# Kernel optimization log

Hardware: AMD Instinct MI355X
Metric: run time of the kernel (lower is better)

Reference implementation:

```python
import jax, jax.numpy as jnp
import numpy as np
from jax import lax

B, N, D, H, T = 32, 128, 512, 512, 31
INI = 0.01


def setup_inputs() -> dict:
    key = jax.random.key(0)
    ks = jax.random.split(key, 16)
    xav_dh = float(np.sqrt(2.0 / (D + H)))
    xav_hh = float(np.sqrt(2.0 / (H + H)))
    u = lambda k, s, a: jax.random.uniform(k, s, jnp.float32, -a, a)
    return {
        "attn_mem": jax.random.normal(ks[0], (B, N, D), jnp.float32),
        "mem_sizes": jax.random.randint(ks[1], (B,), 64, N + 1),
        "lstm_in": jax.random.normal(ks[2], (B, T, D), jnp.float32),
        "init_h": u(ks[3], (1, H), INI),
        "init_c": u(ks[4], (1, H), INI),
        "init_i": u(ks[5], (D,), 0.1),
        "w_ih": jax.random.normal(ks[6], (4 * H, D), jnp.float32) * xav_dh,
        "w_hh": jax.random.normal(ks[7], (4 * H, H), jnp.float32) * xav_hh,
        "b_ih": u(ks[8], (4 * H,), INI),
        "b_hh": u(ks[9], (4 * H,), INI),
        "attn_wm": jax.random.normal(ks[10], (D, H), jnp.float32) * xav_dh,
        "attn_wq": jax.random.normal(ks[11], (H, H), jnp.float32) * xav_hh,
        "attn_v": u(ks[12], (H,), INI),
        "hop_wm": jax.random.normal(ks[13], (D, H), jnp.float32) * xav_dh,
        "hop_wq": jax.random.normal(ks[14], (H, H), jnp.float32) * xav_hh,
        "hop_v": u(ks[15], (H,), INI),
    }


def _attention_score(feat, query, v, w):
    # feat: [B,N,H], query: [B,Tq,H] -> [B,Tq,N]
    q = jnp.einsum("bth,hk->btk", query, w)
    s = jnp.tanh(feat[:, None, :, :] + q[:, :, None, :])  # [B,Tq,N,H]
    return jnp.einsum("btnh,h->btn", s, v)


def _attention(feat, query, v, w, mask):
    score = _attention_score(feat, query, v, w)
    score = jnp.where(mask[:, None, :], score, -1e18)
    norm = jax.nn.softmax(score, axis=-1)
    return jnp.einsum("btn,bnh->bth", norm, feat)


def _lstm(x, h0, c0, w_ih, w_hh, b_ih, b_hh):
    # x: [T,B,D]; h0,c0: [B,H]; pytorch gate order i,f,g,o
    def step(carry, xt):
        h, c = carry
        g = xt @ w_ih.T + h @ w_hh.T + b_ih + b_hh
        i, f, gg, o = jnp.split(g, 4, axis=-1)
        c = jax.nn.sigmoid(f) * c + jax.nn.sigmoid(i) * jnp.tanh(gg)
        h = jax.nn.sigmoid(o) * jnp.tanh(c)
        return (h, c), h
    _, ys = lax.scan(step, (h0, c0), x)
    return ys  # [T,B,H]


def reference(attn_mem, mem_sizes, lstm_in, init_h, init_c, init_i,
              w_ih, w_hh, b_ih, b_hh, attn_wm, attn_wq, attn_v,
              hop_wm, hop_wq, hop_v, n_hop=1):
    bs, n, d = attn_mem.shape
    attn_feat = attn_mem @ attn_wm  # [B,N,H]
    hop_feat = attn_mem @ hop_wm   # [B,N,H]
    h0 = jnp.broadcast_to(init_h[0], (bs, init_h.shape[1]))
    c0 = jnp.broadcast_to(init_c[0], (bs, init_c.shape[1]))
    x = jnp.concatenate([jnp.broadcast_to(init_i, (bs, 1, d)), lstm_in], axis=1)
    query = _lstm(jnp.transpose(x, (1, 0, 2)), h0, c0, w_ih, w_hh, b_ih, b_hh)
    query = jnp.transpose(query, (1, 0, 2))  # [B,Tq,H]
    mask = jnp.arange(n)[None, :] < mem_sizes[:, None]  # [B,N]
    for _ in range(n_hop):
        query = _attention(hop_feat, query, hop_v, hop_wq, mask)
    return _attention_score(attn_feat, query, attn_v, attn_wq)
```

## Files before the change

### kernel.cpp

```cpp
#include <hip/hip_runtime.h>

typedef unsigned short u16;
typedef unsigned int u32;
typedef unsigned long long u64;
typedef __bf16 bf16x8 __attribute__((ext_vector_type(8)));
typedef float f32x4 __attribute__((ext_vector_type(4)));

__device__ __forceinline__ float b2f(u16 u) {
    unsigned int x = ((unsigned int)u) << 16;
    return __builtin_bit_cast(float, x);
}
__device__ __forceinline__ u16 f2b(float f) {
    unsigned int u = __builtin_bit_cast(unsigned int, f);
    unsigned int r = (u + 0x7FFFu + ((u >> 16) & 1u)) >> 16;
    return (u16)r;
}
__device__ __forceinline__ unsigned int pack2(float a, float b) {
    return (unsigned int)f2b(a) | ((unsigned int)f2b(b) << 16);
}
__device__ __forceinline__ float fast_rcp(float x) { return __builtin_amdgcn_rcpf(x); }
__device__ __forceinline__ float fast_tanh(float x) {
    float e = __expf(2.f * x);
    return 1.f - 2.f * fast_rcp(e + 1.f);
}
__device__ __forceinline__ float fast_sig(float x) {
    float e = __expf(-x);
    return fast_rcp(1.f + e);
}

#define FLAG_STRIDE 32

__launch_bounds__(256)
__global__ void k_prep(const float* __restrict__ attn_mem, u16* __restrict__ amem_bf,
                       const float* __restrict__ w_ih, u16* __restrict__ wih_bf,
                       const float* __restrict__ w_hh, u16* __restrict__ whh_bf,
                       const float* __restrict__ lstm_in, const float* __restrict__ init_i,
                       u16* __restrict__ xfull,
                       const float* s0, const float* s1, const float* s2, const float* s3,
                       u16* d0, u16* d1, u16* d2, u16* d3,
                       unsigned int* __restrict__ flags) {
    __shared__ float tile[32][33];
    int bid = blockIdx.x;
    int tid = threadIdx.x;
    if (bid == 0 && tid < 64)
        __hip_atomic_store(&flags[tid * FLAG_STRIDE], 0u, __ATOMIC_RELAXED,
                           __HIP_MEMORY_SCOPE_AGENT);
    if (bid < 4096) {
        const float* s;
        u16* d;
        int i;
        if (bid < 2048) { s = attn_mem; d = amem_bf; i = bid * 256 + tid; }
        else if (bid < 3072) { s = w_ih; d = wih_bf; i = (bid - 2048) * 256 + tid; }
        else { s = w_hh; d = whh_bf; i = (bid - 3072) * 256 + tid; }
        float4 a = ((const float4*)s)[i];
        uint2 p;
        p.x = pack2(a.x, a.y);
        p.y = pack2(a.z, a.w);
        ((uint2*)d)[i] = p;
    } else if (bid < 4608) {
        int idx = (bid - 4096) * 256 + tid;
        int c = idx & 127;
        int t = (idx >> 7) & 31;
        int b = idx >> 12;
        const float4* src = (t == 0) ? ((const float4*)init_i) + c
                                     : ((const float4*)lstm_in) + ((b * 31 + (t - 1)) * 128 + c);
        float4 a = *src;
        uint2 p;
        p.x = pack2(a.x, a.y);
        p.y = pack2(a.z, a.w);
        ((uint2*)xfull)[idx] = p;
    } else {
        int local = bid - 4608;
        int z = local >> 8, rem = local & 255;
        int by = (rem >> 4) * 32, bx = (rem & 15) * 32;
        const float* s;
        u16* d;
        switch (z) {
            case 0: s = s0; d = d0; break;
            case 1: s = s1; d = d1; break;
            case 2: s = s2; d = d2; break;
            default: s = s3; d = d3; break;
        }
        int tx = tid & 31, ty = tid >> 5;
        for (int i = 0; i < 32; i += 8) tile[ty + i][tx] = s[(by + ty + i) * 512 + bx + tx];
        __syncthreads();
        for (int i = 0; i < 32; i += 8) d[(bx + ty + i) * 512 + by + tx] = f2b(tile[tx][ty + i]);
    }
}

__launch_bounds__(256)
__global__ void k_mid(const u16* __restrict__ xfull, const u16* __restrict__ wih,
                      float* __restrict__ xw,
                      const float* __restrict__ b_ih, const float* __restrict__ b_hh,
                      const u16* __restrict__ amem,
                      const u16* __restrict__ WmT_hop, const u16* __restrict__ WmT_attn,
                      u16* __restrict__ hop_feat, u16* __restrict__ attn_feat) {
    __shared__ u16 As[64][40];
    __shared__ u16 Bs[64][40];
    int id = blockIdx.x;
    const u16 *A, *Bt;
    float* Cf = nullptr;
    u16* Cb = nullptr;
    const float *bias1 = nullptr, *bias2 = nullptr;
    int m0, n0, GN;
    if (id < 512) {
        A = xfull; Bt = wih; GN = 2048;
        m0 = (id >> 5) * 64; n0 = (id & 31) * 64;
        Cf = xw; bias1 = b_ih; bias2 = b_hh;
    } else {
        int local = id - 512;
        A = amem; GN = 512;
        if (local < 512) { Bt = WmT_hop; Cb = hop_feat; }
        else { Bt = WmT_attn; Cb = attn_feat; local -= 512; }
        m0 = (local >> 3) * 64; n0 = (local & 7) * 64;
    }
    int tid = threadIdx.x;
    int lane = tid & 63, w = tid >> 6;
    int wm = w >> 1, wn = w & 1;
    int l15 = lane & 15, quad = lane >> 4;
    f32x4 acc[2][2] = {};
    int ar = tid >> 2, ac = (tid & 3) * 8;
    const u16* Ap = A + (m0 + ar) * 512 + ac;
    const u16* Bp = Bt + (n0 + ar) * 512 + ac;
    for (int kt = 0; kt < 16; ++kt) {
        uint4 av = *(const uint4*)(Ap + kt * 32);
        uint4 bv = *(const uint4*)(Bp + kt * 32);
        __syncthreads();
        *(uint4*)&As[ar][ac] = av;
        *(uint4*)&Bs[ar][ac] = bv;
        __syncthreads();
        bf16x8 a0 = *(const bf16x8*)&As[wm * 32 + l15][quad * 8];
        bf16x8 a1 = *(const bf16x8*)&As[wm * 32 + 16 + l15][quad * 8];
        bf16x8 b0 = *(const bf16x8*)&Bs[wn * 32 + l15][quad * 8];
        bf16x8 b1 = *(const bf16x8*)&Bs[wn * 32 + 16 + l15][quad * 8];
        acc[0][0] = __builtin_amdgcn_mfma_f32_16x16x32_bf16(a0, b0, acc[0][0], 0, 0, 0);
        acc[0][1] = __builtin_amdgcn_mfma_f32_16x16x32_bf16(a0, b1, acc[0][1], 0, 0, 0);
        acc[1][0] = __builtin_amdgcn_mfma_f32_16x16x32_bf16(a1, b0, acc[1][0], 0, 0, 0);
        acc[1][1] = __builtin_amdgcn_mfma_f32_16x16x32_bf16(a1, b1, acc[1][1], 0, 0, 0);
    }
    for (int ai = 0; ai < 2; ++ai)
        for (int bi = 0; bi < 2; ++bi) {
            int row = m0 + wm * 32 + ai * 16 + quad * 4;
            int col = n0 + wn * 32 + bi * 16 + l15;
            if (Cb) {
                for (int r = 0; r < 4; ++r) Cb[(row + r) * GN + col] = f2b(acc[ai][bi][r]);
            } else {
                float bias = bias1[col] + bias2[col];
                for (int r = 0; r < 4; ++r) Cf[(row + r) * GN + col] = acc[ai][bi][r] + bias;
            }
        }
}

template <bool BF16OUT>
__launch_bounds__(256)
__global__ void k_gemm(const u16* __restrict__ A, const u16* __restrict__ Bt,
                       void* __restrict__ Cv, int GN,
                       const float* __restrict__ bias1, const float* __restrict__ bias2) {
    __shared__ u16 As[64][40];
    __shared__ u16 Bs[64][40];
    int m0 = blockIdx.y * 64, n0 = blockIdx.x * 64;
    int tid = threadIdx.x;
    int lane = tid & 63, w = tid >> 6;
    int wm = w >> 1, wn = w & 1;
    int l15 = lane & 15, quad = lane >> 4;
    f32x4 acc[2][2] = {};
    int ar = tid >> 2, ac = (tid & 3) * 8;
    const u16* Ap = A + (m0 + ar) * 512 + ac;
    const u16* Bp = Bt + (n0 + ar) * 512 + ac;
    for (int kt = 0; kt < 16; ++kt) {
        uint4 av = *(const uint4*)(Ap + kt * 32);
        uint4 bv = *(const uint4*)(Bp + kt * 32);
        __syncthreads();
        *(uint4*)&As[ar][ac] = av;
        *(uint4*)&Bs[ar][ac] = bv;
        __syncthreads();
        bf16x8 a0 = *(const bf16x8*)&As[wm * 32 + l15][quad * 8];
        bf16x8 a1 = *(const bf16x8*)&As[wm * 32 + 16 + l15][quad * 8];
        bf16x8 b0 = *(const bf16x8*)&Bs[wn * 32 + l15][quad * 8];
        bf16x8 b1 = *(const bf16x8*)&Bs[wn * 32 + 16 + l15][quad * 8];
        acc[0][0] = __builtin_amdgcn_mfma_f32_16x16x32_bf16(a0, b0, acc[0][0], 0, 0, 0);
        acc[0][1] = __builtin_amdgcn_mfma_f32_16x16x32_bf16(a0, b1, acc[0][1], 0, 0, 0);
        acc[1][0] = __builtin_amdgcn_mfma_f32_16x16x32_bf16(a1, b0, acc[1][0], 0, 0, 0);
        acc[1][1] = __builtin_amdgcn_mfma_f32_16x16x32_bf16(a1, b1, acc[1][1], 0, 0, 0);
    }
    for (int ai = 0; ai < 2; ++ai)
        for (int bi = 0; bi < 2; ++bi) {
            int row = m0 + wm * 32 + ai * 16 + quad * 4;
            int col = n0 + wn * 32 + bi * 16 + l15;
            float bias = 0.f;
            if (bias1) bias = bias1[col] + bias2[col];
            if constexpr (BF16OUT) {
                u16* C = (u16*)Cv;
                for (int r = 0; r < 4; ++r) C[(row + r) * GN + col] = f2b(acc[ai][bi][r] + bias);
            } else {
                float* C = (float*)Cv;
                for (int r = 0; r < 4; ++r) C[(row + r) * GN + col] = acc[ai][bi][r] + bias;
            }
        }
}

__launch_bounds__(256, 1)
__global__ void k_lstm4(const u16* __restrict__ w_hh_bf, const float* __restrict__ xw,
                        const float* __restrict__ init_h, const float* __restrict__ init_c,
                        const u16* __restrict__ wq_hop_T, float* __restrict__ qbuf,
                        u64* __restrict__ hbuf, unsigned int* __restrict__ flags) {
    __shared__ u16 Bw[32][520];
    __shared__ u16 Ah[32][520];
    __shared__ float gl[32][33];
    __shared__ u16 gbuf[32][8];
    __shared__ u16 Wq[16][520];
    int tid = threadIdx.x;
    int k0 = blockIdx.x * 8;
    int lane = tid & 63, w = tid >> 6;
    int mi = w >> 1, ni = w & 1;
    int l15 = lane & 15, quad = lane >> 4;
    int row = tid >> 3, seg = tid & 7;
    {
        int j = (row >> 3) * 512 + k0 + (row & 7);
        const uint4* src = (const uint4*)(w_hh_bf + j * 512);
        for (int i = 0; i < 8; ++i)
            *(uint4*)&Bw[row][(seg + 8 * i) * 8] = src[seg + 8 * i];
    }
    if (row < 16) {
        if (row < 8) {
            const uint4* src = (const uint4*)(wq_hop_T + (k0 + row) * 512);
            for (int i = 0; i < 8; ++i)
                *(uint4*)&Wq[row][(seg + 8 * i) * 8] = src[seg + 8 * i];
        } else {
            uint4 z = {0, 0, 0, 0};
            for (int i = 0; i < 8; ++i)
                *(uint4*)&Wq[row][(seg + 8 * i) * 8] = z;
        }
    }
    for (int i = 0; i < 8; ++i) {
        int col = (seg + 8 * i) * 8;
        float4 f0 = *(const float4*)(init_h + col);
        float4 f1 = *(const float4*)(init_h + col + 4);
        uint4 p;
        p.x = pack2(f0.x, f0.y);
        p.y = pack2(f0.z, f0.w);
        p.z = pack2(f1.x, f1.y);
        p.w = pack2(f1.z, f1.w);
        *(uint4*)&Ah[row][col] = p;
    }
    float c = init_c[k0 + seg];
    float xcur0, xcur1, xcur2, xcur3;
    {
        const float* p = xw + (row << 5) * 2048 + k0 + seg;
        xcur0 = p[0]; xcur1 = p[512]; xcur2 = p[1024]; xcur3 = p[1536];
    }
    __syncthreads();
    for (int t = 0; t < 32; ++t) {
        f32x4 acc = {};
#pragma unroll
        for (int kc = 0; kc < 16; ++kc) {
            bf16x8 a = *(const bf16x8*)&Ah[mi * 16 + l15][kc * 32 + quad * 8];
            bf16x8 b = *(const bf16x8*)&Bw[ni * 16 + l15][kc * 32 + quad * 8];
            acc = __builtin_amdgcn_mfma_f32_16x16x32_bf16(a, b, acc, 0, 0, 0);
        }
        {
            int r0 = mi * 16 + quad * 4, col = ni * 16 + l15;
            for (int r = 0; r < 4; ++r) gl[r0 + r][col] = acc[r];
        }
        __syncthreads();
        int b = row, kg = k0 + seg;
        float gi = gl[b][seg] + xcur0;
        float gf = gl[b][8 + seg] + xcur1;
        float gg = gl[b][16 + seg] + xcur2;
        float go = gl[b][24 + seg] + xcur3;
        float cnew = fast_sig(gf) * c + fast_sig(gi) * fast_tanh(gg);
        c = cnew;
        float h = fast_sig(go) * fast_tanh(cnew);
        u16 hb = f2b(h);
        gbuf[b][seg] = hb;
        __syncthreads();
        if (tid < 64) {
            int b2 = tid >> 1, half = tid & 1;
            u64 v = *(const u64*)&gbuf[b2][half * 4];
            u64* dst = hbuf + (t & 1) * 4096 + blockIdx.x * 64 + tid;
            __hip_atomic_store(dst, v, __ATOMIC_RELAXED, __HIP_MEMORY_SCOPE_AGENT);
            __builtin_amdgcn_s_waitcnt(0);
            if (tid == 0)
                __hip_atomic_store(&flags[blockIdx.x * FLAG_STRIDE], (unsigned int)(t + 1),
                                   __ATOMIC_RELAXED, __HIP_MEMORY_SCOPE_AGENT);
            while (true) {
                unsigned int f = __hip_atomic_load(&flags[tid * FLAG_STRIDE],
                                                   __ATOMIC_RELAXED, __HIP_MEMORY_SCOPE_AGENT);
                if (__ballot(f > (unsigned int)t) == ~0ull) break;
                __builtin_amdgcn_s_sleep(1);
            }
        } else if (t > 0 && w <= 2) {
            int mt = w - 1;
            f32x4 acc2 = {};
#pragma unroll
            for (int kc = 0; kc < 16; ++kc) {
                bf16x8 a = *(const bf16x8*)&Ah[mt * 16 + l15][kc * 32 + quad * 8];
                bf16x8 bq = *(const bf16x8*)&Wq[l15][kc * 32 + quad * 8];
                acc2 = __builtin_amdgcn_mfma_f32_16x16x32_bf16(a, bq, acc2, 0, 0, 0);
            }
            if (l15 < 8) {
                int bidx = mt * 16 + quad * 4;
                for (int r = 0; r < 4; ++r)
                    qbuf[(((bidx + r) << 5) + (t - 1)) * 512 + k0 + l15] = acc2[r];
            }
        }
        __syncthreads();
        int tn = (t < 31) ? t + 1 : 31;
        float xn0, xn1, xn2, xn3;
        {
            const float* p = xw + ((row << 5) + tn) * 2048 + k0 + seg;
            xn0 = p[0]; xn1 = p[512]; xn2 = p[1024]; xn3 = p[1536];
        }
        {
            const u64* src = hbuf + (t & 1) * 4096;
#pragma unroll
            for (int i = 0; i < 8; ++i) {
                int bid2 = seg + 8 * i;
                u64 v0 = __hip_atomic_load(&src[bid2 * 64 + row * 2], __ATOMIC_RELAXED,
                                           __HIP_MEMORY_SCOPE_AGENT);
                u64 v1 = __hip_atomic_load(&src[bid2 * 64 + row * 2 + 1], __ATOMIC_RELAXED,
                                           __HIP_MEMORY_SCOPE_AGENT);
                *(u64*)&Ah[row][bid2 * 8] = v0;
                *(u64*)&Ah[row][bid2 * 8 + 4] = v1;
            }
        }
        __syncthreads();
        xcur0 = xn0; xcur1 = xn1; xcur2 = xn2; xcur3 = xn3;
    }
    if (w == 1 || w == 2) {
        int mt = w - 1;
        f32x4 acc2 = {};
#pragma unroll
        for (int kc = 0; kc < 16; ++kc) {
            bf16x8 a = *(const bf16x8*)&Ah[mt * 16 + l15][kc * 32 + quad * 8];
            bf16x8 bq = *(const bf16x8*)&Wq[l15][kc * 32 + quad * 8];
            acc2 = __builtin_amdgcn_mfma_f32_16x16x32_bf16(a, bq, acc2, 0, 0, 0);
        }
        if (l15 < 8) {
            int bidx = mt * 16 + quad * 4;
            for (int r = 0; r < 4; ++r)
                qbuf[(((bidx + r) << 5) + 31) * 512 + k0 + l15] = acc2[r];
        }
    }
}

__launch_bounds__(256)
__global__ void k_hop(const u16* __restrict__ feat, const float* __restrict__ q,
                      const float* __restrict__ v, const int* __restrict__ mem_sizes,
                      u16* __restrict__ nq) {
    __shared__ float qs[512];
    __shared__ float vs[512];
    __shared__ float sc[128];
    __shared__ float ns[128];
    int bt = blockIdx.x;
    int b = bt >> 5;
    int tid = threadIdx.x;
    qs[tid] = q[bt * 512 + tid];
    qs[tid + 256] = q[bt * 512 + 256 + tid];
    vs[tid] = v[tid];
    vs[tid + 256] = v[tid + 256];
    __syncthreads();
    int lane = tid & 63, w = tid >> 6;
    int h0 = lane * 8;
    float qv[8], vv[8];
#pragma unroll
    for (int i = 0; i < 8; ++i) { qv[i] = qs[h0 + i]; vv[i] = vs[h0 + i]; }
    const u16* fb = feat + (size_t)b * 128 * 512;
    for (int i = 0; i < 32; ++i) {
        int n = w * 32 + i;
        uint4 fv = *(const uint4*)(fb + n * 512 + h0);
        float fr[8];
        fr[0] = b2f((u16)(fv.x & 0xFFFF)); fr[1] = b2f((u16)(fv.x >> 16));
        fr[2] = b2f((u16)(fv.y & 0xFFFF)); fr[3] = b2f((u16)(fv.y >> 16));
        fr[4] = b2f((u16)(fv.z & 0xFFFF)); fr[5] = b2f((u16)(fv.z >> 16));
        fr[6] = b2f((u16)(fv.w & 0xFFFF)); fr[7] = b2f((u16)(fv.w >> 16));
        float a = 0.f;
#pragma unroll
        for (int jj = 0; jj < 8; ++jj) a += fast_tanh(fr[jj] + qv[jj]) * vv[jj];
        for (int off = 1; off < 64; off <<= 1) a += __shfl_xor(a, off);
        if (lane == 0) sc[n] = a;
    }
    __syncthreads();
    if (tid < 64) {
        int ms = mem_sizes[b];
        float s0 = (tid < ms) ? sc[tid] : -1e30f;
        float s1 = (tid + 64 < ms) ? sc[tid + 64] : -1e30f;
        float m = fmaxf(s0, s1);
        for (int off = 1; off < 64; off <<= 1) m = fmaxf(m, __shfl_xor(m, off));
        float e0 = __expf(s0 - m), e1 = __expf(s1 - m);
        float s = e0 + e1;
        for (int off = 1; off < 64; off <<= 1) s += __shfl_xor(s, off);
        float r = fast_rcp(s);
        ns[tid] = e0 * r;
        ns[tid + 64] = e1 * r;
    }
    __syncthreads();
    float a0 = 0.f, a1 = 0.f;
    int hc = tid * 2;
    for (int n = 0; n < 128; ++n) {
        float f = ns[n];
        unsigned int pv = *(const unsigned int*)(fb + n * 512 + hc);
        a0 += f * b2f((u16)(pv & 0xFFFF));
        a1 += f * b2f((u16)(pv >> 16));
    }
    ((unsigned int*)nq)[bt * 256 + tid] = pack2(a0, a1);
}

__launch_bounds__(256)
__global__ void k_score(const u16* __restrict__ feat, const float* __restrict__ q,
                        const float* __restrict__ v, float* __restrict__ outp) {
    __shared__ float qs[512];
    __shared__ float vs[512];
    __shared__ float sc[128];
    int bt = blockIdx.x;
    int b = bt >> 5;
    int tid = threadIdx.x;
    qs[tid] = q[bt * 512 + tid];
    qs[tid + 256] = q[bt * 512 + 256 + tid];
    vs[tid] = v[tid];
    vs[tid + 256] = v[tid + 256];
    __syncthreads();
    int lane = tid & 63, w = tid >> 6;
    int h0 = lane * 8;
    float qv[8], vv[8];
#pragma unroll
    for (int i = 0; i < 8; ++i) { qv[i] = qs[h0 + i]; vv[i] = vs[h0 + i]; }
    const u16* fb = feat + (size_t)b * 128 * 512;
    for (int i = 0; i < 32; ++i) {
        int n = w * 32 + i;
        uint4 fv = *(const uint4*)(fb + n * 512 + h0);
        float fr[8];
        fr[0] = b2f((u16)(fv.x & 0xFFFF)); fr[1] = b2f((u16)(fv.x >> 16));
        fr[2] = b2f((u16)(fv.y & 0xFFFF)); fr[3] = b2f((u16)(fv.y >> 16));
        fr[4] = b2f((u16)(fv.z & 0xFFFF)); fr[5] = b2f((u16)(fv.z >> 16));
        fr[6] = b2f((u16)(fv.w & 0xFFFF)); fr[7] = b2f((u16)(fv.w >> 16));
        float a = 0.f;
#pragma unroll
        for (int jj = 0; jj < 8; ++jj) a += fast_tanh(fr[jj] + qv[jj]) * vv[jj];
        for (int off = 1; off < 64; off <<= 1) a += __shfl_xor(a, off);
        if (lane == 0) sc[n] = a;
    }
    __syncthreads();
    if (tid < 128) outp[bt * 128 + tid] = sc[tid];
}

extern "C" void kernel_launch(void* const* d_in, const int* in_sizes, int n_in,
                              void* d_out, int out_size, void* d_ws, size_t ws_size,
                              hipStream_t stream) {
    (void)in_sizes; (void)n_in; (void)out_size; (void)ws_size;
    const float* attn_mem = (const float*)d_in[0];
    const int* mem_sizes = (const int*)d_in[1];
    const float* lstm_in = (const float*)d_in[2];
    const float* init_h = (const float*)d_in[3];
    const float* init_c = (const float*)d_in[4];
    const float* init_i = (const float*)d_in[5];
    const float* w_ih = (const float*)d_in[6];
    const float* w_hh = (const float*)d_in[7];
    const float* b_ih = (const float*)d_in[8];
    const float* b_hh = (const float*)d_in[9];
    const float* attn_wm = (const float*)d_in[10];
    const float* attn_wq = (const float*)d_in[11];
    const float* attn_v = (const float*)d_in[12];
    const float* hop_wm = (const float*)d_in[13];
    const float* hop_wq = (const float*)d_in[14];
    const float* hop_v = (const float*)d_in[15];
    float* out = (float*)d_out;

    char* ws = (char*)d_ws;
    size_t off = 0;
    auto alloc = [&](size_t bytes) {
        void* p = ws + off;
        off += (bytes + 255) & ~(size_t)255;
        return p;
    };
    u16* amem_bf = (u16*)alloc(4096 * 512 * 2);
    u16* xfull_bf = (u16*)alloc(1024 * 512 * 2);
    u16* wih_bf = (u16*)alloc(2048 * 512 * 2);
    u16* whh_bf = (u16*)alloc(2048 * 512 * 2);
    u16* WmT_hop = (u16*)alloc(512 * 512 * 2);
    u16* WmT_attn = (u16*)alloc(512 * 512 * 2);
    u16* WqT_hop = (u16*)alloc(512 * 512 * 2);
    u16* WqT_attn = (u16*)alloc(512 * 512 * 2);
    float* xw = (float*)alloc(1024 * 2048 * 4);
    u16* hop_feat = (u16*)alloc(4096 * 512 * 2);
    u16* attn_feat = (u16*)alloc(4096 * 512 * 2);
    u64* hbuf = (u64*)alloc(2 * 64 * 64 * 8);
    unsigned int* flags = (unsigned int*)alloc(64 * FLAG_STRIDE * 4);
    float* qbuf = (float*)alloc(1024 * 512 * 4);
    u16* nq = (u16*)alloc(1024 * 512 * 2);

    k_prep<<<5632, 256, 0, stream>>>(attn_mem, amem_bf, w_ih, wih_bf, w_hh, whh_bf,
                                     lstm_in, init_i, xfull_bf,
                                     attn_wm, hop_wm, hop_wq, attn_wq,
                                     WmT_attn, WmT_hop, WqT_hop, WqT_attn, flags);
    k_mid<<<1536, 256, 0, stream>>>(xfull_bf, wih_bf, xw, b_ih, b_hh,
                                    amem_bf, WmT_hop, WmT_attn, hop_feat, attn_feat);
    k_lstm4<<<64, 256, 0, stream>>>(whh_bf, xw, init_h, init_c, WqT_hop, qbuf, hbuf, flags);
    k_hop<<<1024, 256, 0, stream>>>(hop_feat, qbuf, hop_v, mem_sizes, nq);
    k_gemm<false><<<dim3(8, 16), 256, 0, stream>>>(nq, WqT_attn, qbuf, 512, nullptr, nullptr);
    k_score<<<1024, 256, 0, stream>>>(attn_feat, qbuf, attn_v, out);
}
```

Measured before the change: 332.5 us.

## Overlap feature GEMMs with LSTM recurrence by merging them into one launch

Moves the hop_feat and attn_feat projection GEMMs out of the pre-LSTM kernel and into the LSTM kernel as 1024 extra blocks beyond the 64 recurrence blocks. The idea is that these independent GEMMs can run on idle CUs while the latency-bound, flag-synchronised LSTM recurrence executes, instead of sitting on the critical path before it. The risk is that the persistent LSTM blocks rely on all 64 being co-resident for their inter-block flags. The extra blocks add shared memory to every block, and if they are scheduled ahead of the LSTM blocks they could delay or deadlock the recurrence.

```diff
diff --git a/kernel.cpp b/kernel.cpp
--- a/kernel.cpp
+++ b/kernel.cpp
@@ -89,39 +89,21 @@
 }
 
 __launch_bounds__(256)
-__global__ void k_mid(const u16* __restrict__ xfull, const u16* __restrict__ wih,
-                      float* __restrict__ xw,
-                      const float* __restrict__ b_ih, const float* __restrict__ b_hh,
-                      const u16* __restrict__ amem,
-                      const u16* __restrict__ WmT_hop, const u16* __restrict__ WmT_attn,
-                      u16* __restrict__ hop_feat, u16* __restrict__ attn_feat) {
+__global__ void k_xw(const u16* __restrict__ xfull, const u16* __restrict__ wih,
+                     float* __restrict__ xw,
+                     const float* __restrict__ b_ih, const float* __restrict__ b_hh) {
     __shared__ u16 As[64][40];
     __shared__ u16 Bs[64][40];
     int id = blockIdx.x;
-    const u16 *A, *Bt;
-    float* Cf = nullptr;
-    u16* Cb = nullptr;
-    const float *bias1 = nullptr, *bias2 = nullptr;
-    int m0, n0, GN;
-    if (id < 512) {
-        A = xfull; Bt = wih; GN = 2048;
-        m0 = (id >> 5) * 64; n0 = (id & 31) * 64;
-        Cf = xw; bias1 = b_ih; bias2 = b_hh;
-    } else {
-        int local = id - 512;
-        A = amem; GN = 512;
-        if (local < 512) { Bt = WmT_hop; Cb = hop_feat; }
-        else { Bt = WmT_attn; Cb = attn_feat; local -= 512; }
-        m0 = (local >> 3) * 64; n0 = (local & 7) * 64;
-    }
+    int m0 = (id >> 5) * 64, n0 = (id & 31) * 64;
     int tid = threadIdx.x;
     int lane = tid & 63, w = tid >> 6;
     int wm = w >> 1, wn = w & 1;
     int l15 = lane & 15, quad = lane >> 4;
     f32x4 acc[2][2] = {};
     int ar = tid >> 2, ac = (tid & 3) * 8;
-    const u16* Ap = A + (m0 + ar) * 512 + ac;
-    const u16* Bp = Bt + (n0 + ar) * 512 + ac;
+    const u16* Ap = xfull + (m0 + ar) * 512 + ac;
+    const u16* Bp = wih + (n0 + ar) * 512 + ac;
     for (int kt = 0; kt < 16; ++kt) {
         uint4 av = *(const uint4*)(Ap + kt * 32);
         uint4 bv = *(const uint4*)(Bp + kt * 32);
@@ -142,20 +124,14 @@
         for (int bi = 0; bi < 2; ++bi) {
             int row = m0 + wm * 32 + ai * 16 + quad * 4;
             int col = n0 + wn * 32 + bi * 16 + l15;
-            if (Cb) {
-                for (int r = 0; r < 4; ++r) Cb[(row + r) * GN + col] = f2b(acc[ai][bi][r]);
-            } else {
-                float bias = bias1[col] + bias2[col];
-                for (int r = 0; r < 4; ++r) Cf[(row + r) * GN + col] = acc[ai][bi][r] + bias;
-            }
-        }
-}
-
-template <bool BF16OUT>
+            float bias = b_ih[col] + b_hh[col];
+            for (int r = 0; r < 4; ++r) xw[(row + r) * 2048 + col] = acc[ai][bi][r] + bias;
+        }
+}
+
 __launch_bounds__(256)
 __global__ void k_gemm(const u16* __restrict__ A, const u16* __restrict__ Bt,
-                       void* __restrict__ Cv, int GN,
-                       const float* __restrict__ bias1, const float* __restrict__ bias2) {
+                       float* __restrict__ C, int GN) {
     __shared__ u16 As[64][40];
     __shared__ u16 Bs[64][40];
     int m0 = blockIdx.y * 64, n0 = blockIdx.x * 64;
@@ -187,29 +163,64 @@
         for (int bi = 0; bi < 2; ++bi) {
             int row = m0 + wm * 32 + ai * 16 + quad * 4;
             int col = n0 + wn * 32 + bi * 16 + l15;
-            float bias = 0.f;
-            if (bias1) bias = bias1[col] + bias2[col];
-            if constexpr (BF16OUT) {
-                u16* C = (u16*)Cv;
-                for (int r = 0; r < 4; ++r) C[(row + r) * GN + col] = f2b(acc[ai][bi][r] + bias);
-            } else {
-                float* C = (float*)Cv;
-                for (int r = 0; r < 4; ++r) C[(row + r) * GN + col] = acc[ai][bi][r] + bias;
-            }
+            for (int r = 0; r < 4; ++r) C[(row + r) * GN + col] = acc[ai][bi][r];
         }
 }
 
 __launch_bounds__(256, 1)
-__global__ void k_lstm4(const u16* __restrict__ w_hh_bf, const float* __restrict__ xw,
+__global__ void k_lstm5(const u16* __restrict__ w_hh_bf, const float* __restrict__ xw,
                         const float* __restrict__ init_h, const float* __restrict__ init_c,
                         const u16* __restrict__ wq_hop_T, float* __restrict__ qbuf,
-                        u64* __restrict__ hbuf, unsigned int* __restrict__ flags) {
+                        u64* __restrict__ hbuf, unsigned int* __restrict__ flags,
+                        const u16* __restrict__ amem_bf,
+                        const u16* __restrict__ WmT_hop, const u16* __restrict__ WmT_attn,
+                        u16* __restrict__ hop_feat, u16* __restrict__ attn_feat) {
     __shared__ u16 Bw[32][520];
     __shared__ u16 Ah[32][520];
     __shared__ float gl[32][33];
     __shared__ u16 gbuf[32][8];
     __shared__ u16 Wq[16][520];
+    __shared__ u16 As[64][40];
+    __shared__ u16 Bs[64][40];
     int tid = threadIdx.x;
+    if (blockIdx.x >= 64) {
+        int local = (int)blockIdx.x - 64;
+        const u16* Bt;
+        u16* C;
+        if (local < 512) { Bt = WmT_hop; C = hop_feat; }
+        else { Bt = WmT_attn; C = attn_feat; local -= 512; }
+        int m0 = (local >> 3) * 64, n0 = (local & 7) * 64;
+        int lane = tid & 63, w = tid >> 6;
+        int wm = w >> 1, wn = w & 1;
+        int l15 = lane & 15, quad = lane >> 4;
+        f32x4 acc[2][2] = {};
+        int ar = tid >> 2, ac = (tid & 3) * 8;
+        const u16* Ap = amem_bf + (m0 + ar) * 512 + ac;
+        const u16* Bp = Bt + (n0 + ar) * 512 + ac;
+        for (int kt = 0; kt < 16; ++kt) {
+            uint4 av = *(const uint4*)(Ap + kt * 32);
+            uint4 bv = *(const uint4*)(Bp + kt * 32);
+            __syncthreads();
+            *(uint4*)&As[ar][ac] = av;
+            *(uint4*)&Bs[ar][ac] = bv;
+            __syncthreads();
+            bf16x8 a0 = *(const bf16x8*)&As[wm * 32 + l15][quad * 8];
+            bf16x8 a1 = *(const bf16x8*)&As[wm * 32 + 16 + l15][quad * 8];
+            bf16x8 b0 = *(const bf16x8*)&Bs[wn * 32 + l15][quad * 8];
+            bf16x8 b1 = *(const bf16x8*)&Bs[wn * 32 + 16 + l15][quad * 8];
+            acc[0][0] = __builtin_amdgcn_mfma_f32_16x16x32_bf16(a0, b0, acc[0][0], 0, 0, 0);
+            acc[0][1] = __builtin_amdgcn_mfma_f32_16x16x32_bf16(a0, b1, acc[0][1], 0, 0, 0);
+            acc[1][0] = __builtin_amdgcn_mfma_f32_16x16x32_bf16(a1, b0, acc[1][0], 0, 0, 0);
+            acc[1][1] = __builtin_amdgcn_mfma_f32_16x16x32_bf16(a1, b1, acc[1][1], 0, 0, 0);
+        }
+        for (int ai = 0; ai < 2; ++ai)
+            for (int bi = 0; bi < 2; ++bi) {
+                int row = m0 + wm * 32 + ai * 16 + quad * 4;
+                int col = n0 + wn * 32 + bi * 16 + l15;
+                for (int r = 0; r < 4; ++r) C[(row + r) * 512 + col] = f2b(acc[ai][bi][r]);
+            }
+        return;
+    }
     int k0 = blockIdx.x * 8;
     int lane = tid & 63, w = tid >> 6;
     int mi = w >> 1, ni = w & 1;
@@ -493,10 +504,10 @@
                                      lstm_in, init_i, xfull_bf,
                                      attn_wm, hop_wm, hop_wq, attn_wq,
                                      WmT_attn, WmT_hop, WqT_hop, WqT_attn, flags);
-    k_mid<<<1536, 256, 0, stream>>>(xfull_bf, wih_bf, xw, b_ih, b_hh,
-                                    amem_bf, WmT_hop, WmT_attn, hop_feat, attn_feat);
-    k_lstm4<<<64, 256, 0, stream>>>(whh_bf, xw, init_h, init_c, WqT_hop, qbuf, hbuf, flags);
+    k_xw<<<512, 256, 0, stream>>>(xfull_bf, wih_bf, xw, b_ih, b_hh);
+    k_lstm5<<<1088, 256, 0, stream>>>(whh_bf, xw, init_h, init_c, WqT_hop, qbuf, hbuf, flags,
+                                      amem_bf, WmT_hop, WmT_attn, hop_feat, attn_feat);
     k_hop<<<1024, 256, 0, stream>>>(hop_feat, qbuf, hop_v, mem_sizes, nq);
-    k_gemm<false><<<dim3(8, 16), 256, 0, stream>>>(nq, WqT_attn, qbuf, 512, nullptr, nullptr);
+    k_gemm<<<dim3(8, 16), 256, 0, stream>>>(nq, WqT_attn, qbuf, 512);
     k_score<<<1024, 256, 0, stream>>>(attn_feat, qbuf, attn_v, out);
 }
```

Result: faster. 322.5 us (-3.0%).
